# Kernel optimization log

Measured on AMD Instinct MI355X. Metric: run time of the kernel, lower is better.

Reference implementation:

```python
import jax, jax.numpy as jnp
import numpy as np

N_LEVELS = 16
LOG2_T = 19
BASE_RES = 256
PER_LEVEL_SCALE = 2.0
PRIME0 = 1
PRIME1 = 2654435761  # spatial hash prime (Instant-NGP)


def setup_inputs() -> dict:
    key = jax.random.key(0)
    k1, k2 = jax.random.split(key)
    B = 1_000_000
    T = 1 << LOG2_T
    F = 2
    x = jax.random.uniform(k1, (B, 2), dtype=jnp.float32)  # coords in [0,1)
    # 16 stacked embedding tables, init uniform(-1e-4, 1e-4) like the torch module
    tables = jax.random.uniform(k2, (N_LEVELS, T, F), dtype=jnp.float32,
                                minval=-1e-4, maxval=1e-4)
    return {"x": x, "tables": tables}


def _forward(x, tables):
    L, T, F = tables.shape
    B = x.shape[0]
    # per-level grid resolutions: int(base * scale**i)
    res = jnp.asarray([int(BASE_RES * PER_LEVEL_SCALE ** i) for i in range(L)],
                      dtype=jnp.float32)  # [L]
    xs = x[None, :, :] * res[:, None, None]          # [L,B,2] scaled coords
    vmin = jnp.floor(xs)                             # [L,B,2]
    w = xs - vmin                                    # bilinear weights [L,B,2]
    # 4 corner offsets in torch module order: [0,0],[0,1],[1,0],[1,1]
    offsets = jnp.array([[0, 0], [0, 1], [1, 0], [1, 1]], dtype=jnp.int32)
    corners = vmin.astype(jnp.int32)[:, :, None, :] + offsets[None, None, :, :]  # [L,B,4,2]
    cu = corners.astype(jnp.uint32)
    # XOR hash with uint32 wraparound (matches torch int32 overflow semantics)
    h = (cu[..., 0] * jnp.uint32(PRIME0)) ^ (cu[..., 1] * jnp.uint32(PRIME1))
    idx = (h & jnp.uint32(T - 1)).astype(jnp.int32)  # [L,B,4]
    # per-level gather of the 4 corner embeddings
    emb = jax.vmap(lambda tbl, i: tbl[i])(tables, idx)  # [L,B,4,F]
    wx = w[..., 0:1]  # [L,B,1]
    wy = w[..., 1:2]
    c0 = emb[:, :, 0] * (1.0 - wx) + emb[:, :, 2] * wx  # interp along dim 0
    c1 = emb[:, :, 1] * (1.0 - wx) + emb[:, :, 3] * wx
    out = c0 * (1.0 - wy) + c1 * wy                     # [L,B,F]
    # torch concatenates level outputs along the feature dim -> [B, L*F]
    return jnp.moveaxis(out, 0, 1).reshape(B, L * F)


def reference(x, tables):
    return _forward(x, tables)
```

## Files before the change

kernel.cpp:

```cpp
#include <hip/hip_runtime.h>
#include <hip/hip_fp16.h>

#define NLEVELS 16
#define LOG2T 19
#define TENTRIES (1u << LOG2T)
#define TMASK (TENTRIES - 1u)
#define PRIME1 2654435761u
#define THREADS 256
#define PTS_PER_THREAD 4
#define PTS_PER_BLOCK (THREADS * PTS_PER_THREAD)

typedef float vf2 __attribute__((ext_vector_type(2)));
typedef float vf4 __attribute__((ext_vector_type(4)));

__global__ __launch_bounds__(256) void cvt_fp16_kernel(
    const vf4* __restrict__ src, uint2* __restrict__ dst, int npair)
{
    int i = blockIdx.x * blockDim.x + threadIdx.x;
    if (i >= npair) return;
    vf4 v = src[i];
    __half2 a = __floats2half2_rn(v.x, v.y);
    __half2 b = __floats2half2_rn(v.z, v.w);
    uint2 o;
    o.x = *reinterpret_cast<unsigned*>(&a);
    o.y = *reinterpret_cast<unsigned*>(&b);
    dst[i] = o;
}

__global__ __launch_bounds__(THREADS) void hashgrid2d_lvl_fp16(
    const float* __restrict__ x,
    const __half2* __restrict__ aux,
    vf2* __restrict__ outT,
    int B, int chunksPerLevel)
{
    int bid  = blockIdx.x;
    int xcd  = bid & 7;
    int seq  = bid >> 3;
    int half = (seq >= chunksPerLevel) ? 1 : 0;
    int level = 2 * xcd + half;
    int chunk = seq - half * chunksPerLevel;

    const __half2* __restrict__ tbl = aux + ((size_t)level << LOG2T);
    const vf2* __restrict__ x2 = reinterpret_cast<const vf2*>(x);
    float res = (float)(256 << level);

    int base = chunk * PTS_PER_BLOCK + (int)threadIdx.x;

    __half2 e00[PTS_PER_THREAD], e01[PTS_PER_THREAD], e10[PTS_PER_THREAD], e11[PTS_PER_THREAD];
    float w0[PTS_PER_THREAD], w1[PTS_PER_THREAD];
    int   bidx[PTS_PER_THREAD];

    #pragma unroll
    for (int k = 0; k < PTS_PER_THREAD; ++k) {
        int b = base + k * THREADS;
        bidx[k] = b;
        if (b >= B) b = B - 1;
        vf2 xy = __builtin_nontemporal_load(&x2[b]);

        float xs0 = xy.x * res;
        float xs1 = xy.y * res;
        float v0 = floorf(xs0), v1 = floorf(xs1);
        w0[k] = xs0 - v0;
        w1[k] = xs1 - v1;

        unsigned i0 = (unsigned)(int)v0;
        unsigned i1 = (unsigned)(int)v1;
        unsigned hy0 = i1 * PRIME1;
        unsigned hy1 = hy0 + PRIME1;

        unsigned idx00 = ( i0       ^ hy0) & TMASK;
        unsigned idx01 = ( i0       ^ hy1) & TMASK;
        unsigned idx10 = ((i0 + 1u) ^ hy0) & TMASK;
        unsigned idx11 = ((i0 + 1u) ^ hy1) & TMASK;

        e00[k] = tbl[idx00];
        e01[k] = tbl[idx01];
        e10[k] = tbl[idx10];
        e11[k] = tbl[idx11];
    }

    #pragma unroll
    for (int k = 0; k < PTS_PER_THREAD; ++k) {
        int b = bidx[k];
        if (b >= B) continue;
        float omw0 = 1.0f - w0[k], omw1 = 1.0f - w1[k];
        float c0x = __low2float(e00[k])  * omw0 + __low2float(e10[k])  * w0[k];
        float c0y = __high2float(e00[k]) * omw0 + __high2float(e10[k]) * w0[k];
        float c1x = __low2float(e01[k])  * omw0 + __low2float(e11[k])  * w0[k];
        float c1y = __high2float(e01[k]) * omw0 + __high2float(e11[k]) * w0[k];
        vf2 o;
        o.x = c0x * omw1 + c1x * w1[k];
        o.y = c0y * omw1 + c1y * w1[k];
        __builtin_nontemporal_store(o, &outT[(size_t)level * B + b]);
    }
}

__global__ __launch_bounds__(THREADS) void transpose_out(
    const vf2* __restrict__ outT, vf2* __restrict__ out, int B)
{
    __shared__ vf2 tile[NLEVELS][THREADS + 1];
    int base = blockIdx.x * THREADS;
    int t = (int)threadIdx.x;

    #pragma unroll
    for (int l = 0; l < NLEVELS; ++l) {
        int b = base + t;
        if (b < B) tile[l][t] = __builtin_nontemporal_load(&outT[(size_t)l * B + b]);
    }
    __syncthreads();

    int l   = t & 15;
    int sub = t >> 4;
    #pragma unroll
    for (int g = 0; g < NLEVELS; ++g) {
        int i = g * 16 + sub;
        int b = base + i;
        if (b < B)
            __builtin_nontemporal_store(tile[l][i], &out[(size_t)b * NLEVELS + l]);
    }
}

__global__ __launch_bounds__(256) void hashgrid2d_fp16(
    const float* __restrict__ x, const __half2* __restrict__ aux,
    float* __restrict__ out, int B)
{
    int tid = blockIdx.x * blockDim.x + threadIdx.x;
    int b = tid >> 4;
    if (b >= B) return;
    int l = tid & 15;
    vf2 xy = __builtin_nontemporal_load(reinterpret_cast<const vf2*>(x) + b);
    float res = (float)(256 << l);
    float xs0 = xy.x * res, xs1 = xy.y * res;
    float v0 = floorf(xs0), v1 = floorf(xs1);
    float w0 = xs0 - v0,    w1 = xs1 - v1;
    unsigned i0 = (unsigned)(int)v0, i1 = (unsigned)(int)v1;
    unsigned hy0 = i1 * PRIME1, hy1 = hy0 + PRIME1;
    unsigned idx00 = ( i0       ^ hy0) & TMASK;
    unsigned idx01 = ( i0       ^ hy1) & TMASK;
    unsigned idx10 = ((i0 + 1u) ^ hy0) & TMASK;
    unsigned idx11 = ((i0 + 1u) ^ hy1) & TMASK;
    const __half2* tbl = aux + ((size_t)l << LOG2T);
    __half2 e00 = tbl[idx00], e01 = tbl[idx01], e10 = tbl[idx10], e11 = tbl[idx11];
    float omw0 = 1.0f - w0, omw1 = 1.0f - w1;
    float c0x = __low2float(e00)  * omw0 + __low2float(e10)  * w0;
    float c0y = __high2float(e00) * omw0 + __high2float(e10) * w0;
    float c1x = __low2float(e01)  * omw0 + __low2float(e11)  * w0;
    float c1y = __high2float(e01) * omw0 + __high2float(e11) * w0;
    vf2 o;
    o.x = c0x * omw1 + c1x * w1;
    o.y = c0y * omw1 + c1y * w1;
    __builtin_nontemporal_store(o, reinterpret_cast<vf2*>(out) + tid);
}

__global__ __launch_bounds__(256) void hashgrid2d_f32(
    const float* __restrict__ x, const float* __restrict__ tables,
    float* __restrict__ out, int B)
{
    int tid = blockIdx.x * blockDim.x + threadIdx.x;
    int b = tid >> 4;
    if (b >= B) return;
    int l = tid & 15;
    vf2 xy = __builtin_nontemporal_load(reinterpret_cast<const vf2*>(x) + b);
    float res = (float)(256 << l);
    float xs0 = xy.x * res, xs1 = xy.y * res;
    float v0 = floorf(xs0), v1 = floorf(xs1);
    float w0 = xs0 - v0,    w1 = xs1 - v1;
    unsigned i0 = (unsigned)(int)v0, i1 = (unsigned)(int)v1;
    unsigned hy0 = i1 * PRIME1, hy1 = hy0 + PRIME1;
    unsigned idx00 = ( i0       ^ hy0) & TMASK;
    unsigned idx01 = ( i0       ^ hy1) & TMASK;
    unsigned idx10 = ((i0 + 1u) ^ hy0) & TMASK;
    unsigned idx11 = ((i0 + 1u) ^ hy1) & TMASK;
    const vf2* tbl = reinterpret_cast<const vf2*>(tables) + ((size_t)l << LOG2T);
    vf2 e00 = tbl[idx00], e01 = tbl[idx01], e10 = tbl[idx10], e11 = tbl[idx11];
    float omw0 = 1.0f - w0, omw1 = 1.0f - w1;
    float c0x = e00.x * omw0 + e10.x * w0;
    float c0y = e00.y * omw0 + e10.y * w0;
    float c1x = e01.x * omw0 + e11.x * w0;
    float c1y = e01.y * omw0 + e11.y * w0;
    vf2 o;
    o.x = c0x * omw1 + c1x * w1;
    o.y = c0y * omw1 + c1y * w1;
    __builtin_nontemporal_store(o, reinterpret_cast<vf2*>(out) + tid);
}

extern "C" void kernel_launch(void* const* d_in, const int* in_sizes, int n_in,
                              void* d_out, int out_size, void* d_ws, size_t ws_size,
                              hipStream_t stream) {
    const float* x      = (const float*)d_in[0];
    const float* tables = (const float*)d_in[1];
    float* out          = (float*)d_out;
    int B = in_sizes[0] / 2;

    const size_t auxBytes  = (size_t)NLEVELS * TENTRIES * 4;
    const size_t outTBytes = (size_t)B * NLEVELS * sizeof(vf2);

    int block = 256;
    int npair = NLEVELS * TENTRIES / 2;
    int cgrid = (npair + block - 1) / block;

    if (ws_size >= auxBytes + outTBytes) {
        __half2* aux = reinterpret_cast<__half2*>(d_ws);
        vf2* outT = reinterpret_cast<vf2*>((char*)d_ws + auxBytes);
        cvt_fp16_kernel<<<cgrid, block, 0, stream>>>(
            reinterpret_cast<const vf4*>(tables), reinterpret_cast<uint2*>(aux), npair);
        int chunksPerLevel = (B + PTS_PER_BLOCK - 1) / PTS_PER_BLOCK;
        int mgrid = NLEVELS * chunksPerLevel;
        hashgrid2d_lvl_fp16<<<mgrid, THREADS, 0, stream>>>(x, aux, outT, B, chunksPerLevel);
        int tgrid = (B + THREADS - 1) / THREADS;
        transpose_out<<<tgrid, THREADS, 0, stream>>>(outT, reinterpret_cast<vf2*>(out), B);
    } else if (ws_size >= auxBytes) {
        __half2* aux = reinterpret_cast<__half2*>(d_ws);
        cvt_fp16_kernel<<<cgrid, block, 0, stream>>>(
            reinterpret_cast<const vf4*>(tables), reinterpret_cast<uint2*>(aux), npair);
        int total = B * NLEVELS;
        int grid  = (total + block - 1) / block;
        hashgrid2d_fp16<<<grid, block, 0, stream>>>(x, aux, out, B);
    } else {
        int total = B * NLEVELS;
        int grid  = (total + block - 1) / block;
        hashgrid2d_f32<<<grid, block, 0, stream>>>(x, tables, out, B);
    }
}
```

Before: 244.0 us.

## Pair adjacent hash-corner loads and store intermediate level outputs as fp16

When the x corner index is even, the two x-adjacent corners hash to neighbouring table slots, so one 8-byte load fetches both and the number of gather requests drops. The intermediate level-major buffer is stored as packed half2 instead of float2, halving its write and read traffic in the gather and transpose kernels. This adds an extra fp16 rounding of the interpolated outputs and a divergent branch between the paired and unpaired paths.

```diff
diff --git a/kernel.cpp b/kernel.cpp
--- a/kernel.cpp
+++ b/kernel.cpp
@@ -27,10 +27,13 @@
     dst[i] = o;
 }
 
-__global__ __launch_bounds__(THREADS) void hashgrid2d_lvl_fp16(
+static __device__ __forceinline__ float h2low(unsigned u)  { __half2 h = *reinterpret_cast<__half2*>(&u); return __low2float(h); }
+static __device__ __forceinline__ float h2high(unsigned u) { __half2 h = *reinterpret_cast<__half2*>(&u); return __high2float(h); }
+
+__global__ __launch_bounds__(THREADS) void hashgrid2d_lvl_fp16m(
     const float* __restrict__ x,
     const __half2* __restrict__ aux,
-    vf2* __restrict__ outT,
+    unsigned* __restrict__ outT,
     int B, int chunksPerLevel)
 {
     int bid  = blockIdx.x;
@@ -40,13 +43,15 @@
     int level = 2 * xcd + half;
     int chunk = seq - half * chunksPerLevel;
 
-    const __half2* __restrict__ tbl = aux + ((size_t)level << LOG2T);
+    const unsigned* __restrict__ tbl1 =
+        reinterpret_cast<const unsigned*>(aux) + ((size_t)level << LOG2T);
+    const uint2* __restrict__ tbl2 = reinterpret_cast<const uint2*>(tbl1);
     const vf2* __restrict__ x2 = reinterpret_cast<const vf2*>(x);
     float res = (float)(256 << level);
 
     int base = chunk * PTS_PER_BLOCK + (int)threadIdx.x;
 
-    __half2 e00[PTS_PER_THREAD], e01[PTS_PER_THREAD], e10[PTS_PER_THREAD], e11[PTS_PER_THREAD];
+    unsigned e00u[PTS_PER_THREAD], e01u[PTS_PER_THREAD], e10u[PTS_PER_THREAD], e11u[PTS_PER_THREAD];
     float w0[PTS_PER_THREAD], w1[PTS_PER_THREAD];
     int   bidx[PTS_PER_THREAD];
 
@@ -68,15 +73,26 @@
         unsigned hy0 = i1 * PRIME1;
         unsigned hy1 = hy0 + PRIME1;
 
-        unsigned idx00 = ( i0       ^ hy0) & TMASK;
-        unsigned idx01 = ( i0       ^ hy1) & TMASK;
-        unsigned idx10 = ((i0 + 1u) ^ hy0) & TMASK;
-        unsigned idx11 = ((i0 + 1u) ^ hy1) & TMASK;
-
-        e00[k] = tbl[idx00];
-        e01[k] = tbl[idx01];
-        e10[k] = tbl[idx10];
-        e11[k] = tbl[idx11];
+        unsigned idx00 = (i0 ^ hy0) & TMASK;
+        unsigned idx01 = (i0 ^ hy1) & TMASK;
+
+        uint2 A = tbl2[idx00 >> 1];
+        uint2 B2 = tbl2[idx01 >> 1];
+
+        unsigned a_sel = idx00 & 1u;
+        unsigned b_sel = idx01 & 1u;
+        e00u[k] = a_sel ? A.y : A.x;
+        e01u[k] = b_sel ? B2.y : B2.x;
+
+        if ((i0 & 1u) == 0u) {
+            e10u[k] = a_sel ? A.x : A.y;
+            e11u[k] = b_sel ? B2.x : B2.y;
+        } else {
+            unsigned idx10 = ((i0 + 1u) ^ hy0) & TMASK;
+            unsigned idx11 = ((i0 + 1u) ^ hy1) & TMASK;
+            e10u[k] = tbl1[idx10];
+            e11u[k] = tbl1[idx11];
+        }
     }
 
     #pragma unroll
@@ -84,21 +100,22 @@
         int b = bidx[k];
         if (b >= B) continue;
         float omw0 = 1.0f - w0[k], omw1 = 1.0f - w1[k];
-        float c0x = __low2float(e00[k])  * omw0 + __low2float(e10[k])  * w0[k];
-        float c0y = __high2float(e00[k]) * omw0 + __high2float(e10[k]) * w0[k];
-        float c1x = __low2float(e01[k])  * omw0 + __low2float(e11[k])  * w0[k];
-        float c1y = __high2float(e01[k]) * omw0 + __high2float(e11[k]) * w0[k];
-        vf2 o;
-        o.x = c0x * omw1 + c1x * w1[k];
-        o.y = c0y * omw1 + c1y * w1[k];
-        __builtin_nontemporal_store(o, &outT[(size_t)level * B + b]);
+        float c0x = h2low(e00u[k])  * omw0 + h2low(e10u[k])  * w0[k];
+        float c0y = h2high(e00u[k]) * omw0 + h2high(e10u[k]) * w0[k];
+        float c1x = h2low(e01u[k])  * omw0 + h2low(e11u[k])  * w0[k];
+        float c1y = h2high(e01u[k]) * omw0 + h2high(e11u[k]) * w0[k];
+        float ox = c0x * omw1 + c1x * w1[k];
+        float oy = c0y * omw1 + c1y * w1[k];
+        __half2 oh = __floats2half2_rn(ox, oy);
+        __builtin_nontemporal_store(*reinterpret_cast<unsigned*>(&oh),
+                                    &outT[(size_t)level * B + b]);
     }
 }
 
 __global__ __launch_bounds__(THREADS) void transpose_out(
-    const vf2* __restrict__ outT, vf2* __restrict__ out, int B)
-{
-    __shared__ vf2 tile[NLEVELS][THREADS + 1];
+    const unsigned* __restrict__ outT, vf2* __restrict__ out, int B)
+{
+    __shared__ unsigned tile[NLEVELS][THREADS + 1];
     int base = blockIdx.x * THREADS;
     int t = (int)threadIdx.x;
 
@@ -115,8 +132,13 @@
     for (int g = 0; g < NLEVELS; ++g) {
         int i = g * 16 + sub;
         int b = base + i;
-        if (b < B)
-            __builtin_nontemporal_store(tile[l][i], &out[(size_t)b * NLEVELS + l]);
+        if (b < B) {
+            unsigned u = tile[l][i];
+            vf2 o;
+            o.x = h2low(u);
+            o.y = h2high(u);
+            __builtin_nontemporal_store(o, &out[(size_t)b * NLEVELS + l]);
+        }
     }
 }
 
@@ -193,7 +215,7 @@
     int B = in_sizes[0] / 2;
 
     const size_t auxBytes  = (size_t)NLEVELS * TENTRIES * 4;
-    const size_t outTBytes = (size_t)B * NLEVELS * sizeof(vf2);
+    const size_t outTBytes = (size_t)B * NLEVELS * sizeof(unsigned);
 
     int block = 256;
     int npair = NLEVELS * TENTRIES / 2;
@@ -201,12 +223,12 @@
 
     if (ws_size >= auxBytes + outTBytes) {
         __half2* aux = reinterpret_cast<__half2*>(d_ws);
-        vf2* outT = reinterpret_cast<vf2*>((char*)d_ws + auxBytes);
+        unsigned* outT = reinterpret_cast<unsigned*>((char*)d_ws + auxBytes);
         cvt_fp16_kernel<<<cgrid, block, 0, stream>>>(
             reinterpret_cast<const vf4*>(tables), reinterpret_cast<uint2*>(aux), npair);
         int chunksPerLevel = (B + PTS_PER_BLOCK - 1) / PTS_PER_BLOCK;
         int mgrid = NLEVELS * chunksPerLevel;
-        hashgrid2d_lvl_fp16<<<mgrid, THREADS, 0, stream>>>(x, aux, outT, B, chunksPerLevel);
+        hashgrid2d_lvl_fp16m<<<mgrid, THREADS, 0, stream>>>(x, aux, outT, B, chunksPerLevel);
         int tgrid = (B + THREADS - 1) / THREADS;
         transpose_out<<<tgrid, THREADS, 0, stream>>>(outT, reinterpret_cast<vf2*>(out), B);
     } else if (ws_size >= auxBytes) {
```

Measured after the change: 274.9 us. 1.13x slower.
